# Performance work log

Measured on AMD Instinct MI355X. Metric: run time of the kernel, lower is better.

## Reference

```python
import jax, jax.numpy as jnp
import numpy as np

H = 512; W = 512; C_IN = 14; HID = 128; N_CELLS = 8192

def _rn(k, shape, sc=0.05):
    return jax.random.normal(k, shape, jnp.float32) * sc

def setup_inputs() -> dict:
    key = jax.random.key(0)
    ks = jax.random.split(key, 32)
    inp = {
        'x': jax.random.normal(ks[0], (1, C_IN, H, W), jnp.float32),
        'cell_i': jax.random.randint(ks[1], (N_CELLS,), 0, H, jnp.int32),
        'cell_j': jax.random.randint(ks[2], (N_CELLS,), 0, W, jnp.int32),
        'action': jax.random.randint(ks[3], (N_CELLS, 4), 0, 2, jnp.int32),
        'w1': _rn(ks[4], (48, C_IN, 3, 3)), 'b1': _rn(ks[5], (48,)),
        'g1': jnp.ones((48,), jnp.float32), 'be1': jnp.zeros((48,), jnp.float32),
        'w2': _rn(ks[6], (96, 48, 3, 3)), 'b2': _rn(ks[7], (96,)),
        'g2': jnp.ones((96,), jnp.float32), 'be2': jnp.zeros((96,), jnp.float32),
        'w3': _rn(ks[8], (HID, 96, 3, 3)), 'b3': _rn(ks[9], (HID,)),
        'g3': jnp.ones((HID,), jnp.float32), 'be3': jnp.zeros((HID,), jnp.float32),
        'fw1': _rn(ks[10], (HID * 9, 256)), 'fb1': _rn(ks[11], (256,)),
        'fw2': _rn(ks[12], (256, 128)), 'fb2': _rn(ks[13], (128,)),
        'bw': _rn(ks[14], (128, 4)), 'bb': _rn(ks[15], (4,)),
        'iw': _rn(ks[16], (128, 4)), 'ib': _rn(ks[17], (4,)),
        'tw': _rn(ks[18], (128, 4)), 'tb': _rn(ks[19], (4,)),
        'vw1': _rn(ks[20], (HID, 64)), 'vb1': _rn(ks[21], (64,)),
        'vw2': _rn(ks[22], (64, 1)), 'vb2': _rn(ks[23], (1,)),
    }
    return inp

def _conv(x, w, b):
    y = jax.lax.conv_general_dilated(x, w, (1, 1), 'SAME',
                                     dimension_numbers=('NCHW', 'OIHW', 'NCHW'))
    return y + b[None, :, None, None]

def _gn(x, gamma, beta, groups, eps=1e-5):
    n, c, h, w = x.shape
    xr = x.reshape(n, groups, -1)
    m = xr.mean(axis=2, keepdims=True)
    v = xr.var(axis=2, keepdims=True)
    xn = ((xr - m) * jax.lax.rsqrt(v + eps)).reshape(n, c, h, w)
    return xn * gamma[None, :, None, None] + beta[None, :, None, None]

def _forward(x, cell_i, cell_j, action, w1, b1, g1, be1, w2, b2, g2, be2,
             w3, b3, g3, be3, fw1, fb1, fw2, fb2, bw, bb, iw, ib, tw, tb,
             vw1, vb1, vw2, vb2):
    # Encoder: conv -> GN -> ReLU x3
    f = jax.nn.relu(_gn(_conv(x, w1, b1), g1, be1, 6))
    f = jax.nn.relu(_gn(_conv(f, w2, b2), g2, be2, 12))
    f = jax.nn.relu(_gn(_conv(f, w3, b3), g3, be3, 16))  # (1, HID, H, W)
    # Value head: global avg pool -> MLP
    pooled = f.mean(axis=(2, 3))  # (1, HID)
    value = jax.nn.relu(pooled @ vw1 + vb1) @ vw2 + vb2  # (1, 1)
    # Per-burning-cell 3x3 patch gather (zero-padded borders)
    fpad = jnp.pad(f, ((0, 0), (0, 0), (1, 1), (1, 1)))[0]  # (HID, H+2, W+2)
    def slice_patch(i, j):
        return jax.lax.dynamic_slice(fpad, (0, i, j), (HID, 3, 3))
    patches = jax.vmap(slice_patch)(cell_i, cell_j)  # (N, HID, 3, 3)
    flat = patches.reshape(patches.shape[0], HID * 9)
    shared = jax.nn.relu(jax.nn.relu(flat @ fw1 + fb1) @ fw2 + fb2)  # (N, 128)
    burn_logits = shared @ bw + bb
    intensity = shared @ iw + ib
    temp = shared @ tw + tb
    p = jnp.clip(jax.nn.sigmoid(burn_logits), 1e-7, 1.0 - 1e-7)
    a = action.astype(jnp.float32)
    log_prob = jnp.sum(a * jnp.log(p) + (1.0 - a) * jnp.log(1.0 - p))
    entropy = -jnp.sum(p * jnp.log(p) + (1.0 - p) * jnp.log(1.0 - p))
    # Scatter sampled actions into grid at N/E/S/W neighbors (in-bounds only)
    di = jnp.array([-1, 0, 1, 0], jnp.int32)
    dj = jnp.array([0, 1, 0, -1], jnp.int32)
    ni = cell_i[:, None] + di
    nj = cell_j[:, None] + dj
    valid = (ni >= 0) & (ni < H) & (nj >= 0) & (nj < W) & (a > 0.5)
    grid = jnp.zeros((H, W), jnp.float32).at[
        jnp.clip(ni, 0, H - 1), jnp.clip(nj, 0, W - 1)].max(valid.astype(jnp.float32))
    return grid, log_prob, entropy, value, intensity, temp

def reference(x, cell_i, cell_j, action, w1, b1, g1, be1, w2, b2, g2, be2,
              w3, b3, g3, be3, fw1, fb1, fw2, fb2, bw, bb, iw, ib, tw, tb,
              vw1, vb1, vw2, vb2):
    return _forward(x, cell_i, cell_j, action, w1, b1, g1, be1, w2, b2, g2, be2,
                    w3, b3, g3, be3, fw1, fb1, fw2, fb2, bw, bb, iw, ib, tw, tb,
                    vw1, vb1, vw2, vb2)
```

## Files before the change

kernel.cpp:

```cpp
#include <hip/hip_runtime.h>
#include <hip/hip_bf16.h>
#include <cstddef>

#define NPIX 262144
#define PW 514
typedef __hip_bfloat16 bf16;
typedef __attribute__((ext_vector_type(8))) short short8;
typedef __attribute__((ext_vector_type(4))) float f32x4;

__device__ inline unsigned short f2bfu(float f){
  __hip_bfloat16 h = __float2bfloat16(f);
  return *(reinterpret_cast<unsigned short*>(&h));
}
__device__ inline float bflo(unsigned u){ return __uint_as_float(u<<16); }
__device__ inline float bfhi(unsigned u){ return __uint_as_float(u & 0xffff0000u); }
__device__ inline unsigned pack2bf(float a, float b){
  unsigned ua = __float_as_uint(a), ub = __float_as_uint(b);
  return ((ua + 0x8000u) >> 16) | ((ub + 0x8000u) & 0xffff0000u);
}
__device__ inline void dma16(const bf16* g, unsigned short* l){
  __builtin_amdgcn_global_load_lds(
      (const __attribute__((address_space(1))) unsigned int*)g,
      (__attribute__((address_space(3))) unsigned int*)l, 16, 0, 0);
}

__device__ inline void computeAB(const float* stats, const float* gamma, const float* beta,
                                 int c, float& A, float& B){
  int g = c >> 3;
  const float invN = 1.f/2097152.f;
  float m = stats[g*2]*invN;
  float v = stats[g*2+1]*invN - m*m;
  float inv = rsqrtf(v + 1e-5f);
  A = inv*gamma[c];
  B = beta[c] - m*A;
}

__global__ void setup_kernel(float* out, float* stats, float* pooled,
                             const float* __restrict__ w1, bf16* __restrict__ wT1,
                             const float* __restrict__ w2, bf16* __restrict__ wT2,
                             const float* __restrict__ w3, bf16* __restrict__ wT3,
                             const float* __restrict__ fw1, bf16* __restrict__ wF1T,
                             const float* __restrict__ fw2, bf16* __restrict__ wF2T){
  int b = blockIdx.x;
  if (b < 1025){
    int i = b*256 + threadIdx.x;
    if (i < 262147) out[i] = 0.f;
    if (i < 68)  stats[i]  = 0.f;
    if (i < 128) pooled[i] = 0.f;
    return;
  }
  b -= 1025;
  if (b < 30){
    int idx = b*256 + threadIdx.x;
    if (idx < 5*48*32){
      int kp = idx & 31; int oc = (idx >> 5) % 48; int kc = idx / (48*32);
      int k = kc*32 + kp;
      int tap = k >> 4, c = k & 15;
      float v = (tap < 9 && c < 14) ? w1[(oc*14 + c)*9 + tap] : 0.f;
      wT1[idx] = __float2bfloat16(v);
    }
    return;
  }
  b -= 30;
  if (b < 216){
    int idx = b*256 + threadIdx.x;
    if (idx < 9*2*96*32){
      int cp = idx & 31; int rest = idx >> 5;
      int oc = rest % 96; rest /= 96;
      int cc = rest % 2; int tap = rest / 2;
      int ic = cc*32 + cp;
      float v = (ic < 48) ? w2[(oc*48 + ic)*9 + tap] : 0.f;
      wT2[idx] = __float2bfloat16(v);
    }
    return;
  }
  b -= 216;
  if (b < 432){
    int idx = b*256 + threadIdx.x;
    if (idx < 9*3*128*32){
      int cp = idx & 31; int rest = idx >> 5;
      int oc = rest & 127; rest >>= 7;
      int cc = rest % 3; int tap = rest / 3;
      int ic = cc*32 + cp;
      float v = (ic < 96) ? w3[(oc*96 + ic)*9 + tap] : 0.f;
      wT3[idx] = __float2bfloat16(v);
    }
    return;
  }
  b -= 432;
  if (b < 1152){
    int idx = b*256 + threadIdx.x;
    if (idx < 36*256*32){
      int kp = idx & 31; int oc = (idx >> 5) & 255; int kc = idx >> 13;
      int k2 = kc*32 + kp;
      int rr = k2 >> 7, ch = k2 & 127;
      wF1T[idx] = __float2bfloat16(fw1[(size_t)(ch*9 + rr)*256 + oc]);
    }
    return;
  }
  b -= 1152;
  {
    int idx = b*256 + threadIdx.x;
    if (idx < 8*128*32){
      int kp = idx & 31; int oc = (idx >> 5) & 127; int kc = idx >> 12;
      wF2T[idx] = __float2bfloat16(fw2[(size_t)(kc*32 + kp)*128 + oc]);
    }
  }
}

__launch_bounds__(256,2)
__global__ void conv1_mfma_kernel(const float* __restrict__ x, const bf16* __restrict__ wT,
                                  const float* __restrict__ bias, bf16* __restrict__ out,
                                  float* __restrict__ stats){
  constexpr int XP = 24;
  __shared__ unsigned short sX[324*XP];
  __shared__ float sStat[96];
  const int tid = threadIdx.x;
  const int lane = tid & 63, wave = tid >> 6;
  const int quad = lane >> 4, l15 = lane & 15;
  const int tileX = (blockIdx.x & 31)*16, tileY = (blockIdx.x >> 5)*16;
  if (tid < 96) sStat[tid] = 0.f;
  for (int p = tid; p < 324; p += 256){ sX[p*XP+14] = 0; sX[p*XP+15] = 0; }
  for (int idx = tid; idx < 14*324; idx += 256){
    int c = idx / 324, p = idx - c*324;
    int r = p / 18, col = p - r*18;
    int gy = tileY + r - 1, gx = tileX + col - 1;
    float v = 0.f;
    if ((unsigned)gy < 512u && (unsigned)gx < 512u) v = x[(size_t)c*NPIX + gy*512 + gx];
    sX[p*XP + c] = f2bfu(v);
  }
  __syncthreads();

  f32x4 acc[3][4];
  #pragma unroll
  for (int t = 0; t < 3; ++t){
    f32x4 bv = *(const f32x4*)(bias + t*16 + quad*4);
    #pragma unroll
    for (int s = 0; s < 4; ++s) acc[t][s] = bv;
  }
  const int pxb = wave*4;
  const int h = quad >> 1, chalf = (quad & 1)*8;
  const int T0[5] = {0,2,4,6,8};
  const int T1[5] = {1,3,5,7,8};
  #pragma unroll
  for (int kc = 0; kc < 5; ++kc){
    short8 a[3];
    #pragma unroll
    for (int t = 0; t < 3; ++t)
      a[t] = *(const short8*)((const unsigned short*)wT + (size_t)(kc*48 + t*16 + l15)*32 + quad*8);
    const int ky = h ? (T1[kc]/3) : (T0[kc]/3);
    const int kx = h ? (T1[kc]%3) : (T0[kc]%3);
    #pragma unroll
    for (int s = 0; s < 4; ++s){
      int py = pxb + s;
      short8 bfr = *(const short8*)(&sX[((py+ky)*18 + l15+kx)*XP + chalf]);
      #pragma unroll
      for (int t = 0; t < 3; ++t)
        acc[t][s] = __builtin_amdgcn_mfma_f32_16x16x32_bf16(a[t], bfr, acc[t][s], 0, 0, 0);
    }
  }
  #pragma unroll
  for (int t = 0; t < 3; ++t){
    #pragma unroll
    for (int r = 0; r < 4; ++r){
      float sv = 0.f, sq = 0.f;
      #pragma unroll
      for (int s = 0; s < 4; ++s){ float v = acc[t][s][r]; sv += v; sq += v*v; }
      #pragma unroll
      for (int m = 1; m < 16; m <<= 1){ sv += __shfl_xor(sv, m); sq += __shfl_xor(sq, m); }
      if (l15 == 0){
        atomicAdd(&sStat[(t*16 + quad*4 + r)*2],   sv);
        atomicAdd(&sStat[(t*16 + quad*4 + r)*2+1], sq);
      }
    }
    #pragma unroll
    for (int s = 0; s < 4; ++s){
      f32x4 v = acc[t][s];
      uint2 pk;
      pk.x = pack2bf(v[0], v[1]);
      pk.y = pack2bf(v[2], v[3]);
      *(uint2*)(out + ((size_t)(tileY+pxb+s+1)*PW + tileX+l15+1)*48 + t*16 + quad*4) = pk;
    }
  }
  __syncthreads();
  if (tid < 12){
    int g = tid >> 1, wsel = tid & 1;
    float v = 0.f;
    #pragma unroll
    for (int j = 0; j < 8; ++j) v += sStat[(g*8+j)*2 + wsel];
    atomicAdd(&stats[g*2 + wsel], v);
  }
}

template<int C>
__global__ void norm_kernel(bf16* buf, const float* __restrict__ stats,
                            const float* __restrict__ gamma, const float* __restrict__ beta){
  __shared__ float sAB[2*C];
  const int tid = threadIdx.x;
  if (tid < C){ float A,B; computeAB(stats, gamma, beta, tid, A, B); sAB[tid]=A; sAB[C+tid]=B; }
  __syncthreads();
  const int y = blockIdx.x >> 2, q = blockIdx.x & 3;
  uint4* row = (uint4*)(buf + (size_t)y*PW*C);
  constexpr int NU4 = PW*C/8/4;
  const bool brow = (y == 0) | (y == 513);
  for (int i = q*NU4 + tid; i < (q+1)*NU4; i += 256){
    int e = i*8;
    int px = e / C;
    if (brow | (px == 0) | (px == 513)){ row[i] = make_uint4(0,0,0,0); continue; }
    int ch = e - px*C;
    uint4 v = row[i];
    unsigned uu[4] = {v.x,v.y,v.z,v.w}, ou[4];
    #pragma unroll
    for (int j = 0; j < 4; ++j){
      float a = fmaxf(bflo(uu[j])*sAB[ch+j*2]   + sAB[C+ch+j*2],   0.f);
      float d = fmaxf(bfhi(uu[j])*sAB[ch+j*2+1] + sAB[C+ch+j*2+1], 0.f);
      ou[j] = pack2bf(a, d);
    }
    row[i] = make_uint4(ou[0],ou[1],ou[2],ou[3]);
  }
}

template<int IC, int NCC, int OCT, int OC>
__launch_bounds__(256, 2)
__global__ void conv_dma_kernel(const bf16* __restrict__ in, const bf16* __restrict__ wT,
                                const float* __restrict__ bias,
                                bf16* __restrict__ out, float* __restrict__ outstats){
  __shared__ unsigned short sIn[2][1296*8];
  __shared__ float sStat[2*OC];
  const int tid  = threadIdx.x;
  const int lane = tid & 63, wave = tid >> 6;
  const int quad = lane >> 4, l15 = lane & 15;
  const int ocg = wave >> 1, pxg = wave & 1;
  const int tileX = (blockIdx.x & 31) * 16, tileY = (blockIdx.x >> 5) * 16;
  const int ocbase = ocg * (OCT*16);

  for (int i = tid; i < 2*OC; i += 256) sStat[i] = 0.f;

  unsigned off[6];
  #pragma unroll
  for (int k = 0; k < 6; ++k){
    int slot = tid + k*256;
    if (k < 5 || tid < 16){
      int row = slot/72; int rem = slot - row*72;
      int cc = rem/18;   int col = rem - cc*18;
      off[k] = (unsigned)(((tileY+row)*PW + tileX+col)*IC + cc*8);
    }
  }
  auto issueDMA = [&](int cr, int bi){
    #pragma unroll
    for (int k = 0; k < 6; ++k){
      if (k == 5 && tid >= 16) continue;
      dma16(in + off[k] + cr*32, &sIn[bi][(tid + k*256)*8]);
    }
  };

  f32x4 acc[OCT][8];
  #pragma unroll
  for (int t = 0; t < OCT; ++t){
    f32x4 bv = *(const f32x4*)(bias + ocbase + t*16 + quad*4);
    #pragma unroll
    for (int s = 0; s < 8; ++s) acc[t][s] = bv;
  }

  issueDMA(0, 0);
  __syncthreads();

  #pragma unroll 1
  for (int cr = 0; cr < NCC; ++cr){
    const unsigned short* B0 = &sIn[cr & 1][(((pxg*8)*4 + quad)*18 + l15)*8];
    const unsigned short* W0 = (const unsigned short*)wT + ((size_t)cr*OC + ocbase + l15)*32 + quad*8;

    #pragma unroll
    for (int tap = 0; tap < 9; ++tap){
      if (tap == 7 && cr + 1 < NCC) issueDMA(cr + 1, (cr + 1) & 1);
      const int ky = tap/3, kx = tap - ky*3;
      short8 a[OCT];
      #pragma unroll
      for (int t = 0; t < OCT; ++t)
        a[t] = *(const short8*)(W0 + (size_t)tap*(NCC*OC*32) + t*512);
      #pragma unroll
      for (int s = 0; s < 8; ++s){
        short8 b = *(const short8*)(B0 + ((s+ky)*72 + kx)*8);
        #pragma unroll
        for (int t = 0; t < OCT; ++t)
          acc[t][s] = __builtin_amdgcn_mfma_f32_16x16x32_bf16(a[t], b, acc[t][s], 0, 0, 0);
      }
    }
    __syncthreads();
  }

  #pragma unroll
  for (int t = 0; t < OCT; ++t){
    #pragma unroll
    for (int r = 0; r < 4; ++r){
      float sv = 0.f, sq = 0.f;
      #pragma unroll
      for (int s = 0; s < 8; ++s){ float v = acc[t][s][r]; sv += v; sq += v*v; }
      #pragma unroll
      for (int m = 1; m < 16; m <<= 1){ sv += __shfl_xor(sv, m); sq += __shfl_xor(sq, m); }
      if (l15 == 0){
        atomicAdd(&sStat[(ocbase + t*16 + quad*4 + r)*2],   sv);
        atomicAdd(&sStat[(ocbase + t*16 + quad*4 + r)*2+1], sq);
      }
    }
    #pragma unroll
    for (int s = 0; s < 8; ++s){
      int py = pxg*8 + s;
      f32x4 v = acc[t][s];
      uint2 pk;
      pk.x = pack2bf(v[0], v[1]);
      pk.y = pack2bf(v[2], v[3]);
      *(uint2*)(out + ((size_t)(tileY+py+1)*PW + (tileX+l15+1))*OC + ocbase + t*16 + quad*4) = pk;
    }
  }
  __syncthreads();
  if (tid < (OC/8)*2){
    int g = tid >> 1, wsel = tid & 1;
    float v = 0.f;
    #pragma unroll
    for (int j = 0; j < 8; ++j) v += sStat[(g*8+j)*2 + wsel];
    atomicAdd(&outstats[g*2 + wsel], v);
  }
}

__launch_bounds__(256)
__global__ void mega_kernel(const bf16* __restrict__ f, const float* __restrict__ instats,
                            const float* __restrict__ gamma, const float* __restrict__ beta,
                            const int* __restrict__ cell_i, const int* __restrict__ cell_j,
                            const int* __restrict__ action,
                            const bf16* __restrict__ wT, const float* __restrict__ fb1,
                            const bf16* __restrict__ wT2, const float* __restrict__ fb2,
                            const float* __restrict__ bw, const float* __restrict__ bb,
                            const float* __restrict__ iw, const float* __restrict__ ib,
                            const float* __restrict__ tw, const float* __restrict__ tb,
                            float* __restrict__ pooled, float* __restrict__ out){
  constexpr int KST = 1160;
  __shared__ unsigned short sG[16*KST];
  __shared__ unsigned short h1L[16*264];
  __shared__ float sAB[256];
  __shared__ int sij[32];
  __shared__ float sRed[2];
  __shared__ float sP[128];
  float* h2L = (float*)sG;
  const int tid = threadIdx.x;
  const int lane = tid & 63, wave = tid >> 6;
  const int quad = lane >> 4, l15 = lane & 15;
  const int cb = blockIdx.x*16;

  if (tid < 2) sRed[tid] = 0.f;
  if (tid < 128){ float A,B; computeAB(instats, gamma, beta, tid, A, B);
    sAB[tid]=A; sAB[128+tid]=B; sP[tid]=0.f; }
  if (tid < 16) sij[tid] = cell_i[cb + tid];
  else if (tid < 32) sij[tid] = cell_j[cb + tid - 16];
  __syncthreads();

  for (int idx = tid; idx < 16*144; idx += 256){
    int c8 = idx & 15; int t2 = idx >> 4;
    int cell = t2 / 9, rr = t2 - cell*9;
    int r = rr/3, cl = rr - r*3;
    int py = sij[cell] + r, px = sij[16+cell] + cl;
    uint4 v = *(const uint4*)(f + ((size_t)py*PW + px)*128 + c8*8);
    bool border = (py==0) | (py==513) | (px==0) | (px==513);
    unsigned uu[4] = {v.x, v.y, v.z, v.w};
    unsigned ou[4];
    #pragma unroll
    for (int j = 0; j < 4; ++j){
      int ch = c8*8 + j*2;
      float a = border ? 0.f : fmaxf(bflo(uu[j])*sAB[ch]   + sAB[128+ch],   0.f);
      float d = border ? 0.f : fmaxf(bfhi(uu[j])*sAB[ch+1] + sAB[128+ch+1], 0.f);
      ou[j] = pack2bf(a, d);
    }
    uint4 wv; wv.x = ou[0]; wv.y = ou[1]; wv.z = ou[2]; wv.w = ou[3];
    *(uint4*)(&sG[cell*KST + rr*128 + c8*8]) = wv;
  }
  __syncthreads();

  {
    f32x4 acc[4];
    const int ocb = wave*64;
    #pragma unroll
    for (int t = 0; t < 4; ++t)
      acc[t] = *(const f32x4*)(fb1 + ocb + t*16 + quad*4);
    #pragma unroll 2
    for (int kc = 0; kc < 36; ++kc){
      short8 b = *(const short8*)(&sG[l15*KST + kc*32 + quad*8]);
      #pragma unroll
      for (int t = 0; t < 4; ++t){
        short8 a = *(const short8*)((const unsigned short*)wT + ((size_t)kc*256 + ocb + t*16 + l15)*32 + quad*8);
        acc[t] = __builtin_amdgcn_mfma_f32_16x16x32_bf16(a, b, acc[t], 0, 0, 0);
      }
    }
    #pragma unroll
    for (int t = 0; t < 4; ++t){
      f32x4 v = acc[t];
      uint2 pk;
      pk.x = pack2bf(fmaxf(v[0],0.f), fmaxf(v[1],0.f));
      pk.y = pack2bf(fmaxf(v[2],0.f), fmaxf(v[3],0.f));
      *(uint2*)(&h1L[l15*264 + ocb + t*16 + quad*4]) = pk;
    }
  }
  __syncthreads();

  {
    const int och = wave*32;
    f32x4 acc2[2];
    #pragma unroll
    for (int t = 0; t < 2; ++t)
      acc2[t] = *(const f32x4*)(fb2 + och + t*16 + quad*4);
    #pragma unroll
    for (int kc = 0; kc < 8; ++kc){
      short8 b = *(const short8*)(&h1L[l15*264 + kc*32 + quad*8]);
      #pragma unroll
      for (int t = 0; t < 2; ++t){
        short8 a = *(const short8*)((const unsigned short*)wT2 + ((size_t)kc*128 + och + t*16 + l15)*32 + quad*8);
        acc2[t] = __builtin_amdgcn_mfma_f32_16x16x32_bf16(a, b, acc2[t], 0, 0, 0);
      }
    }
    #pragma unroll
    for (int t = 0; t < 2; ++t){
      f32x4 v = acc2[t];
      #pragma unroll
      for (int r = 0; r < 4; ++r) v[r] = fmaxf(v[r], 0.f);
      *(f32x4*)(&h2L[l15*132 + och + t*16 + quad*4]) = v;
    }
  }
  __syncthreads();

  if (tid < 192){
    int cell = tid/12, jj = tid - cell*12;
    int which = jj >> 2, o = jj & 3;
    const float* W  = (which==0) ? bw : (which==1 ? iw : tw);
    const float* Bp = (which==0) ? bb : (which==1 ? ib : tb);
    float d = Bp[o];
    const float* h2 = &h2L[cell*132];
    for (int k = 0; k < 128; k++) d += h2[k]*W[k*4+o];
    int cellg = cb + cell;
    if (which == 1){
      out[262147 + cellg*4 + o] = d;
    } else if (which == 2){
      out[262147 + 32768 + cellg*4 + o] = d;
    } else {
      float p = 1.f/(1.f + __expf(-d));
      p = fminf(fmaxf(p, 1e-7f), 1.f - 1e-7f);
      int a = action[cellg*4 + o];
      float lp  = a ? __logf(p) : __logf(1.f-p);
      float ent = -(p*__logf(p) + (1.f-p)*__logf(1.f-p));
      atomicAdd(&sRed[0], lp);
      atomicAdd(&sRed[1], ent);
      if (a){
        const int di[4] = {-1,0,1,0};
        const int dj[4] = {0,1,0,-1};
        int ni = sij[cell] + di[o];
        int nj = sij[16+cell] + dj[o];
        if ((unsigned)ni < 512u && (unsigned)nj < 512u)
          out[ni*512 + nj] = 1.0f;
      }
    }
  }

  {
    const int gl = tid & 15, xl = tid >> 4;
    float A[8], B[8];
    #pragma unroll
    for (int j = 0; j < 8; ++j){ A[j] = sAB[gl*8+j]; B[j] = sAB[128+gl*8+j]; }
    const int y = blockIdx.x;
    float ps[8] = {0,0,0,0,0,0,0,0};
    for (int x2 = xl; x2 < 512; x2 += 16){
      uint4 v = *(const uint4*)(f + ((size_t)(y+1)*PW + x2+1)*128 + gl*8);
      unsigned uu[4] = {v.x, v.y, v.z, v.w};
      #pragma unroll
      for (int j = 0; j < 4; ++j){
        ps[j*2]   += fmaxf(bflo(uu[j])*A[j*2]   + B[j*2],   0.f);
        ps[j*2+1] += fmaxf(bfhi(uu[j])*A[j*2+1] + B[j*2+1], 0.f);
      }
    }
    #pragma unroll
    for (int j = 0; j < 8; ++j) atomicAdd(&sP[gl*8+j], ps[j]);
  }
  __syncthreads();
  if (tid == 0){
    atomicAdd(&out[262144], sRed[0]);
    atomicAdd(&out[262145], sRed[1]);
  }
  if (tid < 128) atomicAdd(&pooled[tid], sP[tid]);
}

__global__ void value_kernel(const float* __restrict__ pooled, const float* __restrict__ vw1,
                             const float* __restrict__ vb1, const float* __restrict__ vw2,
                             const float* __restrict__ vb2, float* __restrict__ out){
  int t = threadIdx.x;
  float h = vb1[t];
  const float invN = 1.f/262144.f;
  for (int c = 0; c < 128; c++) h += (pooled[c]*invN)*vw1[c*64+t];
  h = fmaxf(h, 0.f);
  float v = h*vw2[t];
  #pragma unroll
  for (int off = 32; off; off >>= 1) v += __shfl_xor(v, off);
  if (t == 0) out[262146] = v + vb2[0];
}

extern "C" void kernel_launch(void* const* d_in, const int* in_sizes, int n_in,
                              void* d_out, int out_size, void* d_ws, size_t ws_size,
                              hipStream_t stream) {
  (void)in_sizes; (void)n_in; (void)out_size; (void)ws_size;
  const float* x      = (const float*)d_in[0];
  const int*  cell_i  = (const int*)d_in[1];
  const int*  cell_j  = (const int*)d_in[2];
  const int*  action  = (const int*)d_in[3];
  const float* w1 = (const float*)d_in[4];  const float* b1 = (const float*)d_in[5];
  const float* g1 = (const float*)d_in[6];  const float* be1= (const float*)d_in[7];
  const float* w2 = (const float*)d_in[8];  const float* b2 = (const float*)d_in[9];
  const float* g2 = (const float*)d_in[10]; const float* be2= (const float*)d_in[11];
  const float* w3 = (const float*)d_in[12]; const float* b3 = (const float*)d_in[13];
  const float* g3 = (const float*)d_in[14]; const float* be3= (const float*)d_in[15];
  const float* fw1= (const float*)d_in[16]; const float* fb1= (const float*)d_in[17];
  const float* fw2= (const float*)d_in[18]; const float* fb2= (const float*)d_in[19];
  const float* bw = (const float*)d_in[20]; const float* bb = (const float*)d_in[21];
  const float* iw = (const float*)d_in[22]; const float* ib = (const float*)d_in[23];
  const float* tw = (const float*)d_in[24]; const float* tb = (const float*)d_in[25];
  const float* vw1= (const float*)d_in[26]; const float* vb1= (const float*)d_in[27];
  const float* vw2= (const float*)d_in[28]; const float* vb2= (const float*)d_in[29];

  float* out = (float*)d_out;
  char* ws = (char*)d_ws;
  bf16* buf1 = (bf16*)(ws);
  bf16* buf2 = (bf16*)(ws + 25362816);
  bf16* bufF = (bf16*)(ws + 76088448);
  bf16* wT2  = (bf16*)(ws + 143722624);
  bf16* wT3  = (bf16*)(ws + 143833216);
  bf16* wT1  = (bf16*)(ws + 144054400);
  bf16* wF1T = (bf16*)(ws + 144069760);
  bf16* wF2T = (bf16*)(ws + 144659584);
  float* statsf = (float*)(ws + 144725120);
  float* pooled = statsf + 128;

  setup_kernel<<<2983, 256, 0, stream>>>(out, statsf, pooled, w1, wT1, w2, wT2, w3, wT3,
                                         fw1, wF1T, fw2, wF2T);
  conv1_mfma_kernel<<<1024, 256, 0, stream>>>(x, wT1, b1, buf1, statsf + 0);
  norm_kernel<48><<<514*4, 256, 0, stream>>>(buf1, statsf + 0, g1, be1);
  conv_dma_kernel<48,2,3,96><<<1024, 256, 0, stream>>>(buf1, wT2, b2, buf2, statsf + 12);
  norm_kernel<96><<<514*4, 256, 0, stream>>>(buf2, statsf + 12, g2, be2);
  conv_dma_kernel<96,3,4,128><<<1024, 256, 0, stream>>>(buf2, wT3, b3, bufF, statsf + 36);
  mega_kernel<<<512, 256, 0, stream>>>(bufF, statsf + 36, g3, be3, cell_i, cell_j, action,
                                       wF1T, fb1, wF2T, fb2, bw, bb, iw, ib, tw, tb,
                                       pooled, out);
  value_kernel<<<1, 64, 0, stream>>>(pooled, vw1, vb1, vw2, vb2, out);
}
```

Measured before the change: 357.8 us.

## Retile DMA conv: 8-row tiles, waves split by output channel, reuse input rows across ky

The middle and last conv kernels now use 16x8 pixel tiles instead of 16x16, with twice as many blocks. Each wave owns a slice of output channels over the whole tile instead of half the tile's pixels. The tap loop is reordered so that each input row read from LDS feeds all three kernel rows (ky), cutting LDS reads per MFMA. The prefetch of the next channel chunk moves to the start of each iteration, and launch bounds now ask for 3 blocks per SM. In exchange, the 2-row halo is a larger share of each smaller tile, and each wave loads more weight fragments.

```diff
diff --git a/kernel.cpp b/kernel.cpp
--- a/kernel.cpp
+++ b/kernel.cpp
@@ -220,27 +220,31 @@
   }
 }
 
-template<int IC, int NCC, int OCT, int OC>
-__launch_bounds__(256, 2)
+template<int IC, int NCC, int OCT, int OC, int NW, int TH>
+__launch_bounds__(NW*64, 3)
 __global__ void conv_dma_kernel(const bf16* __restrict__ in, const bf16* __restrict__ wT,
                                 const float* __restrict__ bias,
                                 bf16* __restrict__ out, float* __restrict__ outstats){
-  __shared__ unsigned short sIn[2][1296*8];
+  constexpr int NT   = NW*64;
+  constexpr int ROWS = TH + 2;
+  constexpr int SLOTS = ROWS * 72;
+  constexpr int K    = (SLOTS + NT - 1) / NT;
+  constexpr int REM  = SLOTS - (K-1)*NT;
+  __shared__ unsigned short sIn[2][SLOTS*8];
   __shared__ float sStat[2*OC];
   const int tid  = threadIdx.x;
   const int lane = tid & 63, wave = tid >> 6;
   const int quad = lane >> 4, l15 = lane & 15;
-  const int ocg = wave >> 1, pxg = wave & 1;
-  const int tileX = (blockIdx.x & 31) * 16, tileY = (blockIdx.x >> 5) * 16;
-  const int ocbase = ocg * (OCT*16);
-
-  for (int i = tid; i < 2*OC; i += 256) sStat[i] = 0.f;
-
-  unsigned off[6];
-  #pragma unroll
-  for (int k = 0; k < 6; ++k){
-    int slot = tid + k*256;
-    if (k < 5 || tid < 16){
+  const int tileX = (blockIdx.x & 31) * 16, tileY = (blockIdx.x >> 5) * TH;
+  const int ocbase = wave * (OCT*16);
+
+  for (int i = tid; i < 2*OC; i += NT) sStat[i] = 0.f;
+
+  unsigned off[K];
+  #pragma unroll
+  for (int k = 0; k < K; ++k){
+    int slot = tid + k*NT;
+    if (k < K-1 || tid < REM){
       int row = slot/72; int rem = slot - row*72;
       int cc = rem/18;   int col = rem - cc*18;
       off[k] = (unsigned)(((tileY+row)*PW + tileX+col)*IC + cc*8);
@@ -248,18 +252,18 @@
   }
   auto issueDMA = [&](int cr, int bi){
     #pragma unroll
-    for (int k = 0; k < 6; ++k){
-      if (k == 5 && tid >= 16) continue;
-      dma16(in + off[k] + cr*32, &sIn[bi][(tid + k*256)*8]);
+    for (int k = 0; k < K; ++k){
+      if (k == K-1 && tid >= REM) continue;
+      dma16(in + off[k] + cr*32, &sIn[bi][(tid + k*NT)*8]);
     }
   };
 
-  f32x4 acc[OCT][8];
+  f32x4 acc[OCT][TH];
   #pragma unroll
   for (int t = 0; t < OCT; ++t){
     f32x4 bv = *(const f32x4*)(bias + ocbase + t*16 + quad*4);
     #pragma unroll
-    for (int s = 0; s < 8; ++s) acc[t][s] = bv;
+    for (int s = 0; s < TH; ++s) acc[t][s] = bv;
   }
 
   issueDMA(0, 0);
@@ -267,23 +271,30 @@
 
   #pragma unroll 1
   for (int cr = 0; cr < NCC; ++cr){
-    const unsigned short* B0 = &sIn[cr & 1][(((pxg*8)*4 + quad)*18 + l15)*8];
+    if (cr + 1 < NCC) issueDMA(cr + 1, (cr + 1) & 1);
+    const unsigned short* B0 = &sIn[cr & 1][(quad*18 + l15)*8];
     const unsigned short* W0 = (const unsigned short*)wT + ((size_t)cr*OC + ocbase + l15)*32 + quad*8;
 
     #pragma unroll
-    for (int tap = 0; tap < 9; ++tap){
-      if (tap == 7 && cr + 1 < NCC) issueDMA(cr + 1, (cr + 1) & 1);
-      const int ky = tap/3, kx = tap - ky*3;
-      short8 a[OCT];
-      #pragma unroll
-      for (int t = 0; t < OCT; ++t)
-        a[t] = *(const short8*)(W0 + (size_t)tap*(NCC*OC*32) + t*512);
-      #pragma unroll
-      for (int s = 0; s < 8; ++s){
-        short8 b = *(const short8*)(B0 + ((s+ky)*72 + kx)*8);
+    for (int kx = 0; kx < 3; ++kx){
+      short8 a[3][OCT];
+      #pragma unroll
+      for (int ky = 0; ky < 3; ++ky)
         #pragma unroll
         for (int t = 0; t < OCT; ++t)
-          acc[t][s] = __builtin_amdgcn_mfma_f32_16x16x32_bf16(a[t], b, acc[t][s], 0, 0, 0);
+          a[ky][t] = *(const short8*)(W0 + (size_t)(ky*3+kx)*(NCC*OC*32) + t*512);
+      #pragma unroll
+      for (int r = 0; r < ROWS; ++r){
+        short8 b = *(const short8*)(B0 + (r*72 + kx)*8);
+        #pragma unroll
+        for (int ky = 0; ky < 3; ++ky){
+          const int s = r - ky;
+          if (s >= 0 && s < TH){
+            #pragma unroll
+            for (int t = 0; t < OCT; ++t)
+              acc[t][s] = __builtin_amdgcn_mfma_f32_16x16x32_bf16(a[ky][t], b, acc[t][s], 0, 0, 0);
+          }
+        }
       }
     }
     __syncthreads();
@@ -295,7 +306,7 @@
     for (int r = 0; r < 4; ++r){
       float sv = 0.f, sq = 0.f;
       #pragma unroll
-      for (int s = 0; s < 8; ++s){ float v = acc[t][s][r]; sv += v; sq += v*v; }
+      for (int s = 0; s < TH; ++s){ float v = acc[t][s][r]; sv += v; sq += v*v; }
       #pragma unroll
       for (int m = 1; m < 16; m <<= 1){ sv += __shfl_xor(sv, m); sq += __shfl_xor(sq, m); }
       if (l15 == 0){
@@ -304,13 +315,12 @@
       }
     }
     #pragma unroll
-    for (int s = 0; s < 8; ++s){
-      int py = pxg*8 + s;
+    for (int s = 0; s < TH; ++s){
       f32x4 v = acc[t][s];
       uint2 pk;
       pk.x = pack2bf(v[0], v[1]);
       pk.y = pack2bf(v[2], v[3]);
-      *(uint2*)(out + ((size_t)(tileY+py+1)*PW + (tileX+l15+1))*OC + ocbase + t*16 + quad*4) = pk;
+      *(uint2*)(out + ((size_t)(tileY+s+1)*PW + (tileX+l15+1))*OC + ocbase + t*16 + quad*4) = pk;
     }
   }
   __syncthreads();
@@ -538,9 +548,9 @@
                                          fw1, wF1T, fw2, wF2T);
   conv1_mfma_kernel<<<1024, 256, 0, stream>>>(x, wT1, b1, buf1, statsf + 0);
   norm_kernel<48><<<514*4, 256, 0, stream>>>(buf1, statsf + 0, g1, be1);
-  conv_dma_kernel<48,2,3,96><<<1024, 256, 0, stream>>>(buf1, wT2, b2, buf2, statsf + 12);
+  conv_dma_kernel<48,2,2,96,3,8><<<2048, 192, 0, stream>>>(buf1, wT2, b2, buf2, statsf + 12);
   norm_kernel<96><<<514*4, 256, 0, stream>>>(buf2, statsf + 12, g2, be2);
-  conv_dma_kernel<96,3,4,128><<<1024, 256, 0, stream>>>(buf2, wT3, b3, bufF, statsf + 36);
+  conv_dma_kernel<96,3,2,128,4,8><<<2048, 256, 0, stream>>>(buf2, wT3, b3, bufF, statsf + 36);
   mega_kernel<<<512, 256, 0, stream>>>(bufF, statsf + 36, g3, be3, cell_i, cell_j, action,
                                        wF1T, fb1, wF2T, fb2, bw, bb, iw, ib, tw, tb,
                                        pooled, out);
```

After: 361.2 us. About the same (+0.9%).
